# Kernel tuning notes

Measured on AMD Instinct MI355X. Metric: run time of the kernel, lower is better.

Reference implementation:

```python
import jax, jax.numpy as jnp
import numpy as np
import math

EPS_LN = 1e-5
TARGET_ACTIVITY = 0.1
THETA = 2.0 ** 16

B, NH, T, D, N = 2, 12, 2048, 768, 256


def layernorm(x):
    m = jnp.mean(x, axis=-1, keepdims=True)
    v = jnp.mean((x - m) ** 2, axis=-1, keepdims=True)
    return (x - m) / jnp.sqrt(v + EPS_LN)


def get_freqs(n):
    q = jnp.floor(jnp.arange(n, dtype=jnp.float32) / 2.0) * 2.0  # quantize by 2
    return 1.0 / (THETA ** (q / n)) / (2.0 * math.pi)


def rope(phases, v):
    ph = (phases % 1.0) * (2.0 * math.pi)
    c, s = jnp.cos(ph), jnp.sin(ph)
    even = v[..., 0::2]
    odd = v[..., 1::2]
    v_rot = jnp.stack((-odd, even), axis=-1).reshape(v.shape)  # interleaved rotate
    return v * c + v_rot * s


def setup_inputs() -> dict:
    key = jax.random.key(0)
    ks = jax.random.split(key, 5)
    std = 0.02
    return {
        "x": jax.random.normal(ks[0], (B, 1, T, D), dtype=jnp.float32),
        "encoder": jax.random.normal(ks[1], (NH, D, N), dtype=jnp.float32) * std,
        "encoder_v": jax.random.normal(ks[2], (NH, D, N), dtype=jnp.float32) * std,
        "decoder": jax.random.normal(ks[3], (NH * N, D), dtype=jnp.float32) * std,
        "scale": jnp.ones((D,), dtype=jnp.float32),
        "running_activity": jnp.ones((D,), dtype=jnp.float32) * TARGET_ACTIVITY,
    }


def reference(x, encoder, encoder_v, decoder, scale, running_activity):
    Bv, _, Tv, Dv = x.shape
    nh, _, Nv = encoder.shape

    # encode + ReLU sparsify: [B,1,T,D] @ [nh,D,N] -> [B,nh,T,N]
    x_latent = jnp.einsum('bztd,hdn->bhtn', x, encoder)
    x_sparse = jax.nn.relu(x_latent)

    # RoPE on Q=K=x_sparse
    freqs = get_freqs(Nv)  # [N]
    r_phases = jnp.arange(Tv, dtype=jnp.float32)[:, None] * freqs[None, :]  # [T,N]
    QR = rope(r_phases, x_sparse)
    KR = rope(r_phases, x_sparse)

    # non-softmax causal attention, strictly lower-triangular (diag=-1)
    scores = jnp.einsum('bhtn,bhsn->bhts', QR, KR)
    mask = jnp.tril(jnp.ones((Tv, Tv), dtype=scores.dtype), k=-1)
    scores = scores * mask
    yKV = jnp.einsum('bhts,bsd->bhtd', scores, x[:, 0])  # V = x

    yKV = layernorm(yKV)
    y_sparse = jax.nn.relu(jnp.einsum('bhtd,hdn->bhtn', yKV, encoder_v))
    xy_sparse = x_sparse * y_sparse  # [B,nh,T,N]; dropout=0 (eval)

    # [B,nh,T,N] -> [B,1,T,nh*N] @ [nh*N,D]
    flat = jnp.transpose(xy_sparse, (0, 2, 1, 3)).reshape(Bv, 1, Tv, nh * Nv)
    yMLP = flat @ decoder

    y = layernorm(yMLP)
    regulation = TARGET_ACTIVITY / (running_activity + 1e-6)
    y = y * jnp.sqrt(regulation) * scale

    return layernorm(x + y), xy_sparse
```

## Files before the change

### kernel.cpp

```cpp
#include <hip/hip_runtime.h>
#include <math.h>

#define TT 2048
#define DD 768
#define NN 256
#define NHH 12
#define BB 2
#define CH 512

typedef unsigned short u16;
typedef __attribute__((ext_vector_type(8))) short bf16x8;
typedef __attribute__((ext_vector_type(8))) unsigned short u16x8;
typedef __attribute__((ext_vector_type(4))) float f32x4;

static inline int imin(int a, int b) { return a < b ? a : b; }

__device__ __forceinline__ u16 f2b(float f) {
  union { float f; unsigned u; } a; a.f = f;
  unsigned r = a.u + 0x7FFF + ((a.u >> 16) & 1);
  return (u16)(r >> 16);
}
__device__ __forceinline__ float b2f(u16 h) {
  union { unsigned u; float f; } a; a.u = ((unsigned)h) << 16;
  return a.f;
}

__device__ __forceinline__ void async16(const void* g, void* l) {
  __builtin_amdgcn_global_load_lds(
      (const __attribute__((address_space(1))) unsigned*)g,
      (__attribute__((address_space(3))) unsigned*)l, 16, 0, 0);
}

__device__ __forceinline__ void stage128x32(
    const u16* __restrict__ gbase, size_t ld, u16* lds, int tid) {
  const int w = tid >> 6, l = tid & 63;
  const int r = l >> 2, kc = (l & 3) << 3;
#pragma unroll
  for (int q = 0; q < 2; ++q) {
    const int row0 = w * 32 + q * 16;
    async16(gbase + (size_t)(row0 + r) * ld + kc, lds + row0 * 32);
  }
}

__device__ __forceinline__ void stage64x32(
    const u16* __restrict__ gbase, size_t ld, u16* lds, int tid) {
  const int w = tid >> 6, l = tid & 63;
  const int r = w * 16 + (l >> 2), kc = (l & 3) << 3;
  async16(gbase + (size_t)r * ld + kc, lds + w * 512);
}

__device__ __forceinline__ void mfma_step(
    const u16* As, const u16* Bs, int wr, int wc, int lane, f32x4 acc[4][4]) {
  const int m16 = lane & 15, quad = lane >> 4;
  bf16x8 a[4], b[4];
#pragma unroll
  for (int i = 0; i < 4; ++i)
    a[i] = *(const bf16x8*)&As[(wr * 64 + i * 16 + m16) * 32 + quad * 8];
#pragma unroll
  for (int j = 0; j < 4; ++j)
    b[j] = *(const bf16x8*)&Bs[(wc * 64 + j * 16 + m16) * 32 + quad * 8];
#pragma unroll
  for (int i = 0; i < 4; ++i)
#pragma unroll
    for (int j = 0; j < 4; ++j)
      acc[i][j] = __builtin_amdgcn_mfma_f32_16x16x32_bf16(a[i], b[j], acc[i][j], 0, 0, 0);
}

__device__ __forceinline__ void copy_out128(
    const u16* buf, u16* g, size_t ld, int tid) {
#pragma unroll
  for (int s = 0; s < 8; ++s) {
    const int off = (s * 256 + tid) * 8;
    const int row = off >> 7, col = off & 127;
    *(u16x8*)&g[(size_t)row * ld + col] = *(const u16x8*)&buf[off];
  }
}

#define GEMM_PROLOGUE()                                            \
  __shared__ __attribute__((aligned(16))) u16 smem[16384];         \
  const int tid = threadIdx.x;                                     \
  const int w = tid >> 6, lane = tid & 63;                         \
  const int wr = w >> 1, wc = w & 1;                               \
  const int col16 = lane & 15, quad = lane >> 4;                   \
  f32x4 acc[4][4];                                                 \
  _Pragma("unroll") for (int i = 0; i < 4; ++i)                    \
  _Pragma("unroll") for (int j = 0; j < 4; ++j)                    \
      acc[i][j] = (f32x4){0.f, 0.f, 0.f, 0.f};

#define PIPELINED_K_LOOP(ABASE, ALD, BBASE, BLD, KTOT)                      \
  {                                                                         \
    u16* bA_ = smem; u16* bB_ = smem + 8192;                                \
    stage128x32((ABASE), (ALD), bA_, tid);                                  \
    stage128x32((BBASE), (BLD), bA_ + 4096, tid);                           \
    const int nk_ = (KTOT) / 32;                                            \
    for (int kp_ = 0; kp_ < nk_; ++kp_) {                                   \
      u16* cb_ = (kp_ & 1) ? bB_ : bA_;                                     \
      u16* nb_ = (kp_ & 1) ? bA_ : bB_;                                     \
      if (kp_ + 1 < nk_) {                                                  \
        const int kn_ = (kp_ + 1) * 32;                                     \
        stage128x32((ABASE) + kn_, (ALD), nb_, tid);                        \
        stage128x32((BBASE) + kn_, (BLD), nb_ + 4096, tid);                 \
        asm volatile("s_waitcnt vmcnt(4)" ::: "memory");                    \
      } else {                                                              \
        asm volatile("s_waitcnt vmcnt(0)" ::: "memory");                    \
      }                                                                     \
      __builtin_amdgcn_s_barrier();                                         \
      __builtin_amdgcn_sched_barrier(0);                                    \
      mfma_step(cb_, cb_ + 4096, wr, wc, lane, acc);                        \
      __builtin_amdgcn_sched_barrier(0);                                    \
      __builtin_amdgcn_s_barrier();                                         \
    }                                                                       \
  }

__global__ __launch_bounds__(256) void cvt_bf16(
    const float* __restrict__ in, u16* __restrict__ out, size_t n4) {
  size_t i = ((size_t)blockIdx.x * 256 + threadIdx.x) * 4;
  if (i >= n4 * 4) return;
  float4 v = *(const float4*)&in[i];
  u16 o[4] = {f2b(v.x), f2b(v.y), f2b(v.z), f2b(v.w)};
  *(ushort4*)&out[i] = *(ushort4*)o;
}

__global__ __launch_bounds__(256) void tcvt_bf16(
    const float* __restrict__ in, u16* __restrict__ out, int R, int C,
    size_t inStride, size_t outStride) {
  __shared__ float tile[32][33];
  const float* ip = in + (size_t)blockIdx.z * inStride;
  u16* op = out + (size_t)blockIdx.z * outStride;
  const int c0 = blockIdx.x * 32, r0 = blockIdx.y * 32;
  const int tx = threadIdx.x & 31, ty = threadIdx.x >> 5;
#pragma unroll
  for (int p = 0; p < 4; ++p)
    tile[ty + p * 8][tx] = ip[(size_t)(r0 + ty + p * 8) * C + c0 + tx];
  __syncthreads();
#pragma unroll
  for (int p = 0; p < 4; ++p)
    op[(size_t)(c0 + ty + p * 8) * R + r0 + tx] = f2b(tile[tx][ty + p * 8]);
}

__global__ __launch_bounds__(256) void k_colsum(
    const u16* __restrict__ encvt, float* __restrict__ colsum) {
  const int row = blockIdx.x * 4 + (threadIdx.x >> 6);
  const int lane = threadIdx.x & 63;
  const u16* pr = encvt + (size_t)row * DD;
  float s = 0.f;
#pragma unroll
  for (int i = 0; i < 3; ++i) {
    ushort4 v = *(const ushort4*)&pr[(lane << 2) + i * 256];
    s += b2f(v.x) + b2f(v.y) + b2f(v.z) + b2f(v.w);
  }
#pragma unroll
  for (int off = 32; off; off >>= 1) s += __shfl_xor(s, off);
  if (lane == 0) colsum[row] = s;
}

__global__ __launch_bounds__(256) void k_cstab(float2* __restrict__ cs) {
  const int idx = blockIdx.x * 256 + threadIdx.x;
  const int t = idx >> 7, n2 = idx & 127;
  const float freq = exp2f((float)(2 * n2) * -0.0625f) * 0.15915494309189535f;
  const float phase = (float)t * freq;
  const float ph = (phase - floorf(phase)) * 6.283185307179586f;
  cs[idx] = make_float2(__cosf(ph), __sinf(ph));
}

__global__ __launch_bounds__(256) void k1_encode(
    const u16* __restrict__ x16, const u16* __restrict__ enct,
    const float2* __restrict__ CS,
    u16* __restrict__ qr16, u16* __restrict__ qrt16) {
  const int h = blockIdx.z;
  const int m0 = blockIdx.x * 128, n0 = blockIdx.y * 128;
  GEMM_PROLOGUE();
  PIPELINED_K_LOOP(x16 + (size_t)m0 * DD, DD,
                   enct + ((size_t)h * NN + n0) * DD, DD, DD);
  __syncthreads();
#pragma unroll
  for (int i = 0; i < 4; ++i)
#pragma unroll
    for (int j = 0; j < 4; ++j) {
      const int n = n0 + wc * 64 + j * 16 + col16;
      float rv[4], pv[4];
#pragma unroll
      for (int r = 0; r < 4; ++r) rv[r] = fmaxf(acc[i][j][r], 0.f);
#pragma unroll
      for (int r = 0; r < 4; ++r) pv[r] = __shfl_xor(rv[r], 1);
#pragma unroll
      for (int r = 0; r < 4; ++r) {
        const int lrow = wr * 64 + i * 16 + quad * 4 + r;
        const int t = (m0 + lrow) & (TT - 1);
        const float2 cs = CS[t * 128 + (n >> 1)];
        const float o = (n & 1) ? (rv[r] * cs.x + pv[r] * cs.y)
                                : (rv[r] * cs.x - pv[r] * cs.y);
        smem[lrow * 128 + wc * 64 + j * 16 + col16] = f2b(o);
      }
    }
  __syncthreads();
  const int bq = m0 >> 11, tb = m0 & (TT - 1);
  const size_t sl = (size_t)(bq * NHH + h);
  copy_out128(smem, qr16 + (sl * TT + tb) * NN + n0, NN, tid);
#pragma unroll
  for (int s = 0; s < 8; ++s) {
    const int off = (s * 256 + tid) * 8;
    const int nr = off >> 7, tc = off & 127;
    u16 vals[8];
#pragma unroll
    for (int k = 0; k < 8; ++k) vals[k] = smem[(tc + k) * 128 + nr];
    *(u16x8*)&qrt16[(sl * NN + n0 + nr) * TT + tb + tc] = *(u16x8*)vals;
  }
}

__global__ __launch_bounds__(256) void kS_band(
    const u16* __restrict__ qr16, u16* __restrict__ sb, int bh0) {
  const int z = blockIdx.y;
  const int bh = bh0 + z;
  const int cc = blockIdx.x / 10, rr = blockIdx.x % 10;
  int i = (int)((sqrtf(8.f * rr + 1.f) - 1.f) * 0.5f);
  while ((i + 1) * (i + 2) / 2 <= rr) ++i;
  while (i * (i + 1) / 2 > rr) --i;
  const int j = rr - i * (i + 1) / 2;
  const int t0 = (cc * 4 + i) * 128;
  const int s0 = cc * CH + j * 128;
  const u16* q = qr16 + (size_t)bh * TT * NN;
  GEMM_PROLOGUE();
  PIPELINED_K_LOOP(q + (size_t)t0 * NN, NN, q + (size_t)s0 * NN, NN, NN);
  const bool diag = (i == j);
  __syncthreads();
#pragma unroll
  for (int ii = 0; ii < 4; ++ii)
#pragma unroll
    for (int jj = 0; jj < 4; ++jj) {
      const int s = s0 + wc * 64 + jj * 16 + col16;
#pragma unroll
      for (int r = 0; r < 4; ++r) {
        const int lrow = wr * 64 + ii * 16 + quad * 4 + r;
        const int t = t0 + lrow;
        float v = acc[ii][jj][r];
        if (diag && s >= t) v = 0.f;
        smem[lrow * 128 + wc * 64 + jj * 16 + col16] = f2b(v);
      }
    }
  __syncthreads();
  copy_out128(smem, sb + ((size_t)z * TT + t0) * CH + j * 128, CH, tid);
}

__global__ __launch_bounds__(256) void kB_all(
    const u16* __restrict__ xt16, const u16* __restrict__ qrt16,
    u16* __restrict__ h16, int bh0) {
  __shared__ __attribute__((aligned(16))) u16 sm[20480];
  u16* buf0 = sm;
  u16* buf1 = sm + 6144;
  u16* snap = sm + 12288;
  const int tid = threadIdx.x;
  const int w = tid >> 6, lane = tid & 63;
  const int m16 = lane & 15, quad = lane >> 4;
  const int z = blockIdx.z;
  const int bh = bh0 + z, b = bh / NHH;
  const int d0 = blockIdx.x * 64, n0 = blockIdx.y * 128;
  f32x4 acc[4][2];
#pragma unroll
  for (int i = 0; i < 4; ++i)
#pragma unroll
    for (int j = 0; j < 2; ++j) acc[i][j] = (f32x4){0.f, 0.f, 0.f, 0.f};
  const u16* Ab = xt16 + ((size_t)b * DD + d0) * TT;
  const u16* Bb = qrt16 + ((size_t)bh * NN + n0) * TT;
  for (int c = 0; c < 3; ++c) {
    const int kbase = c * CH;
    stage64x32(Ab + kbase, TT, buf0, tid);
    stage128x32(Bb + kbase, TT, buf0 + 2048, tid);
    for (int s = 0; s < CH / 32; ++s) {
      u16* cb = (s & 1) ? buf1 : buf0;
      u16* nb = (s & 1) ? buf0 : buf1;
      if (s + 1 < CH / 32) {
        const int kn = kbase + (s + 1) * 32;
        stage64x32(Ab + kn, TT, nb, tid);
        stage128x32(Bb + kn, TT, nb + 2048, tid);
        asm volatile("s_waitcnt vmcnt(3)" ::: "memory");
      } else {
        asm volatile("s_waitcnt vmcnt(0)" ::: "memory");
      }
      __builtin_amdgcn_s_barrier();
      __builtin_amdgcn_sched_barrier(0);
      bf16x8 a[4], bb[2];
#pragma unroll
      for (int i = 0; i < 4; ++i)
        a[i] = *(const bf16x8*)&cb[(i * 16 + m16) * 32 + quad * 8];
#pragma unroll
      for (int j = 0; j < 2; ++j)
        bb[j] = *(const bf16x8*)&cb[2048 + (w * 32 + j * 16 + m16) * 32 + quad * 8];
#pragma unroll
      for (int i = 0; i < 4; ++i)
#pragma unroll
        for (int j = 0; j < 2; ++j)
          acc[i][j] = __builtin_amdgcn_mfma_f32_16x16x32_bf16(a[i], bb[j], acc[i][j], 0, 0, 0);
      __builtin_amdgcn_sched_barrier(0);
      __builtin_amdgcn_s_barrier();
    }
#pragma unroll
    for (int i = 0; i < 4; ++i)
#pragma unroll
      for (int j = 0; j < 2; ++j)
#pragma unroll
        for (int r = 0; r < 4; ++r)
          snap[(i * 16 + quad * 4 + r) * 128 + w * 32 + j * 16 + m16] =
              f2b(acc[i][j][r]);
    __syncthreads();
    u16* hd = h16 + (size_t)(z * 3 + c) * DD * NN;
#pragma unroll
    for (int s4 = 0; s4 < 4; ++s4) {
      const int off = (s4 * 256 + tid) * 8;
      const int row = off >> 7, col = off & 127;
      *(u16x8*)&hd[(size_t)(d0 + row) * NN + n0 + col] = *(const u16x8*)&snap[off];
    }
    __syncthreads();
  }
}

__device__ static const int TTORD[16] = {15, 11, 7, 14, 10, 6, 13, 9,
                                         5, 3, 12, 8, 4, 2, 1, 0};

__global__ __launch_bounds__(256) void kA_attn(
    const u16* __restrict__ qr16, const u16* __restrict__ h16,
    const u16* __restrict__ sb, const u16* __restrict__ xt16,
    u16* __restrict__ ykv16, int bh0) {
  __shared__ __attribute__((aligned(16))) u16 smem[32768];
  const int tid = threadIdx.x;
  const int w = tid >> 6, lane = tid & 63;
  const int wr = w >> 1, wc = w & 1;
  const int col16 = lane & 15, quad = lane >> 4;
  const int nwg = gridDim.x;
  const int bid = blockIdx.x;
  const int qq = nwg >> 3, r8 = nwg & 7;
  const int xcd = bid & 7, pos = bid >> 3;
  const int wg = (xcd < r8 ? xcd * (qq + 1) : r8 * (qq + 1) + (xcd - r8) * qq) + pos;
  const int z = wg / 96;
  const int tt = TTORD[(wg / 6) & 15];
  const int d0 = (wg % 6) * 128;
  const int bh = bh0 + z, b = bh / NHH;
  const int c = tt >> 2, it = tt & 3;
  const int t0 = tt * 128;
  f32x4 acc[4][4];
#pragma unroll
  for (int i = 0; i < 4; ++i)
#pragma unroll
    for (int j = 0; j < 4; ++j) acc[i][j] = (f32x4){0.f, 0.f, 0.f, 0.f};

  const int c4 = (c > 0) ? 4 : 0;
  const int nP = c4 + (it + 1) * 2;
  const u16* hs = h16 + ((size_t)(z * 3 + (c > 0 ? c - 1 : 0)) * DD + d0) * NN;
  const u16* qb = qr16 + ((size_t)bh * TT + t0) * NN;
  const u16* sbb = sb + ((size_t)z * TT + t0) * CH;
  const u16* xb = xt16 + ((size_t)b * DD + d0) * TT + c * CH;

#define KA_STAGE(buf, p)                                                  \
  {                                                                       \
    const u16 *pa_, *pb_; size_t la_, lb_;                                \
    if ((p) < c4) {                                                       \
      pa_ = qb + (p) * 64; la_ = NN;                                      \
      pb_ = hs + (p) * 64; lb_ = NN;                                      \
    } else {                                                              \
      const int q_ = (p) - c4;                                            \
      const int j_ = q_ >> 1, kk_ = (q_ & 1) << 6;                        \
      pa_ = sbb + j_ * 128 + kk_; la_ = CH;                               \
      pb_ = xb + j_ * 128 + kk_; lb_ = TT;                                \
    }                                                                     \
    stage128x32(pa_, la_, (buf), tid);                                    \
    stage128x32(pa_ + 32, la_, (buf) + 4096, tid);                        \
    stage128x32(pb_, lb_, (buf) + 8192, tid);                             \
    stage128x32(pb_ + 32, lb_, (buf) + 12288, tid);                       \
  }

  u16* bufA = smem;
  u16* bufB = smem + 16384;
  KA_STAGE(bufA, 0);
  for (int p = 0; p < nP; ++p) {
    u16* cb = (p & 1) ? bufB : bufA;
    u16* nb = (p & 1) ? bufA : bufB;
    if (p + 1 < nP) {
      KA_STAGE(nb, p + 1);
      asm volatile("s_waitcnt vmcnt(8)" ::: "memory");
    } else {
      asm volatile("s_waitcnt vmcnt(0)" ::: "memory");
    }
    __builtin_amdgcn_s_barrier();
    __builtin_amdgcn_sched_barrier(0);
    mfma_step(cb, cb + 8192, wr, wc, lane, acc);
    mfma_step(cb + 4096, cb + 12288, wr, wc, lane, acc);
    __builtin_amdgcn_sched_barrier(0);
    __builtin_amdgcn_s_barrier();
  }
#undef KA_STAGE

  __syncthreads();
#pragma unroll
  for (int i = 0; i < 4; ++i)
#pragma unroll
    for (int j = 0; j < 4; ++j)
#pragma unroll
      for (int r = 0; r < 4; ++r) {
        const int lrow = wr * 64 + i * 16 + quad * 4 + r;
        smem[lrow * 128 + wc * 64 + j * 16 + col16] = f2b(acc[i][j][r]);
      }
  __syncthreads();
  copy_out128(smem, ykv16 + ((size_t)z * TT + t0) * DD + d0, DD, tid);
}

__global__ __launch_bounds__(256) void k3_stats(
    const u16* __restrict__ ykv16, float* __restrict__ mu, float* __restrict__ rs) {
  const int row = blockIdx.x * 4 + (threadIdx.x >> 6);
  const int lane = threadIdx.x & 63;
  const u16* p = ykv16 + (size_t)row * DD;
  float sum = 0.f, sq = 0.f;
#pragma unroll
  for (int i = 0; i < 3; ++i) {
    ushort4 v = *(const ushort4*)&p[(lane << 2) + i * 256];
    float f0 = b2f(v.x), f1 = b2f(v.y), f2 = b2f(v.z), f3 = b2f(v.w);
    sum += f0 + f1 + f2 + f3;
    sq += f0 * f0 + f1 * f1 + f2 * f2 + f3 * f3;
  }
#pragma unroll
  for (int off = 32; off; off >>= 1) {
    sum += __shfl_xor(sum, off);
    sq += __shfl_xor(sq, off);
  }
  if (lane == 0) {
    float m = sum * (1.f / 768.f);
    float v = sq * (1.f / 768.f) - m * m;
    mu[row] = m;
    rs[row] = rsqrtf(v + 1e-5f);
  }
}

__global__ __launch_bounds__(256) void k4_xy(
    const u16* __restrict__ ykv16, const u16* __restrict__ encvt,
    const float2* __restrict__ CS,
    u16* __restrict__ qrxy, const float* __restrict__ mu,
    const float* __restrict__ rs, const float* __restrict__ colsum,
    float* __restrict__ out2, int bh0) {
  const int z = blockIdx.z;
  const int bh = bh0 + z, h = bh % NHH;
  const int t0 = blockIdx.x * 128, n0 = blockIdx.y * 128;
  GEMM_PROLOGUE();
  PIPELINED_K_LOOP(ykv16 + ((size_t)z * TT + t0) * DD, DD,
                   encvt + ((size_t)h * NN + n0) * DD, DD, DD);
  __syncthreads();
#pragma unroll
  for (int i = 0; i < 4; ++i) {
    float muv[4], rsv[4];
#pragma unroll
    for (int r = 0; r < 4; ++r) {
      const int lrow = z * TT + t0 + wr * 64 + i * 16 + quad * 4 + r;
      muv[r] = mu[lrow];
      rsv[r] = rs[lrow];
    }
#pragma unroll
    for (int j = 0; j < 4; ++j) {
      const int n = n0 + wc * 64 + j * 16 + col16;
      const float csum = colsum[h * NN + n];
#pragma unroll
      for (int r = 0; r < 4; ++r) {
        const int lrow = wr * 64 + i * 16 + quad * 4 + r;
        const int t = t0 + lrow;
        const float ys = fmaxf(rsv[r] * acc[i][j][r] - rsv[r] * muv[r] * csum, 0.f);
        const size_t gi = ((size_t)bh * TT + t) * NN + n;
        const unsigned pq = *(const unsigned*)&qrxy[gi & ~(size_t)1];
        const float lo = b2f((u16)pq), hi = b2f((u16)(pq >> 16));
        const float2 cs = CS[t * 128 + (n >> 1)];
        const float xs = (n & 1) ? (hi * cs.x - lo * cs.y)
                                 : (lo * cs.x + hi * cs.y);
        const float val = ys * xs;
        out2[gi] = val;
        smem[lrow * 128 + wc * 64 + j * 16 + col16] = f2b(val);
      }
    }
  }
  __syncthreads();
  copy_out128(smem, qrxy + ((size_t)bh * TT + t0) * NN + n0, NN, tid);
}

__global__ __launch_bounds__(256) void k5_mlp(
    const u16* __restrict__ xyq, const u16* __restrict__ dect,
    float* __restrict__ ymlp) {
  __shared__ __attribute__((aligned(16))) u16 sm[16384];
  u16* buf0 = sm;
  u16* buf1 = sm + 8192;
  const int tid = threadIdx.x;
  const int w = tid >> 6, lane = tid & 63;
  const int wr = w >> 1, wc = w & 1;
  const int m16 = lane & 15, quad = lane >> 4;
  const int m0 = blockIdx.x * 64, d0 = blockIdx.y * 64;
  f32x4 acc[2][2];
#pragma unroll
  for (int i = 0; i < 2; ++i)
#pragma unroll
    for (int j = 0; j < 2; ++j) acc[i][j] = (f32x4){0.f, 0.f, 0.f, 0.f};
  const int ar = w * 16 + (lane >> 2);
  const int m = m0 + ar;
  const int b = m >> 11, t = m & (TT - 1);
  const int kc = (lane & 3) << 3;
#define K5_STAGE(buf, k0)                                                   \
  {                                                                         \
    const int hh_ = (k0) >> 8;                                              \
    const int kk_ = ((k0) & 255) + kc;                                      \
    const u16* ap_ = xyq + ((size_t)(b * NHH + hh_) * TT + t) * NN;         \
    async16(ap_ + kk_, (buf) + w * 512);                                    \
    async16(ap_ + kk_ + 32, (buf) + 2048 + w * 512);                        \
    stage64x32(dect + (size_t)d0 * (NHH * NN) + (k0), NHH * NN,             \
               (buf) + 4096, tid);                                          \
    stage64x32(dect + (size_t)d0 * (NHH * NN) + (k0) + 32, NHH * NN,        \
               (buf) + 6144, tid);                                          \
  }
  const int NK = (NHH * NN) / 64;
  K5_STAGE(buf0, 0);
  for (int s = 0; s < NK; ++s) {
    u16* cb = (s & 1) ? buf1 : buf0;
    u16* nb = (s & 1) ? buf0 : buf1;
    if (s + 1 < NK) {
      K5_STAGE(nb, (s + 1) * 64);
      asm volatile("s_waitcnt vmcnt(4)" ::: "memory");
    } else {
      asm volatile("s_waitcnt vmcnt(0)" ::: "memory");
    }
    __builtin_amdgcn_s_barrier();
    __builtin_amdgcn_sched_barrier(0);
#pragma unroll
    for (int half = 0; half < 2; ++half) {
      bf16x8 a[2], bb[2];
#pragma unroll
      for (int i = 0; i < 2; ++i)
        a[i] = *(const bf16x8*)&cb[half * 2048 + (wr * 32 + i * 16 + m16) * 32 + quad * 8];
#pragma unroll
      for (int j = 0; j < 2; ++j)
        bb[j] = *(const bf16x8*)&cb[4096 + half * 2048 + (wc * 32 + j * 16 + m16) * 32 + quad * 8];
#pragma unroll
      for (int i = 0; i < 2; ++i)
#pragma unroll
        for (int j = 0; j < 2; ++j)
          acc[i][j] = __builtin_amdgcn_mfma_f32_16x16x32_bf16(a[i], bb[j], acc[i][j], 0, 0, 0);
    }
    __builtin_amdgcn_sched_barrier(0);
    __builtin_amdgcn_s_barrier();
  }
#undef K5_STAGE
#pragma unroll
  for (int i = 0; i < 2; ++i)
#pragma unroll
    for (int j = 0; j < 2; ++j) {
      const int d = d0 + wc * 32 + j * 16 + m16;
#pragma unroll
      for (int r = 0; r < 4; ++r) {
        const int mm = m0 + wr * 32 + i * 16 + quad * 4 + r;
        ymlp[(size_t)mm * DD + d] = acc[i][j][r];
      }
    }
}

__global__ __launch_bounds__(256) void k6_final(
    const float* __restrict__ ymlp, const float* __restrict__ x,
    const float* __restrict__ scale, const float* __restrict__ ra,
    float* __restrict__ out1) {
  const int row = blockIdx.x;
  const int tid = threadIdx.x;
  const int wid = tid >> 6, lane = tid & 63;
  __shared__ float red[8];
  float v[3];
  float sum = 0.f, sq = 0.f;
#pragma unroll
  for (int j = 0; j < 3; ++j) {
    v[j] = ymlp[(size_t)row * DD + tid + j * 256];
    sum += v[j]; sq += v[j] * v[j];
  }
#pragma unroll
  for (int off = 32; off; off >>= 1) { sum += __shfl_xor(sum, off); sq += __shfl_xor(sq, off); }
  if (lane == 0) { red[wid] = sum; red[4 + wid] = sq; }
  __syncthreads();
  sum = red[0] + red[1] + red[2] + red[3];
  sq = red[4] + red[5] + red[6] + red[7];
  const float m1 = sum * (1.f / 768.f);
  const float r1 = rsqrtf(sq * (1.f / 768.f) - m1 * m1 + 1e-5f);
  float z[3];
  float sum2 = 0.f, sq2 = 0.f;
#pragma unroll
  for (int j = 0; j < 3; ++j) {
    const int d = tid + j * 256;
    float y = (v[j] - m1) * r1 * sqrtf(0.1f / (ra[d] + 1e-6f)) * scale[d];
    z[j] = x[(size_t)row * DD + d] + y;
    sum2 += z[j]; sq2 += z[j] * z[j];
  }
  __syncthreads();
#pragma unroll
  for (int off = 32; off; off >>= 1) { sum2 += __shfl_xor(sum2, off); sq2 += __shfl_xor(sq2, off); }
  if (lane == 0) { red[wid] = sum2; red[4 + wid] = sq2; }
  __syncthreads();
  sum2 = red[0] + red[1] + red[2] + red[3];
  sq2 = red[4] + red[5] + red[6] + red[7];
  const float m2 = sum2 * (1.f / 768.f);
  const float r2 = rsqrtf(sq2 * (1.f / 768.f) - m2 * m2 + 1e-5f);
#pragma unroll
  for (int j = 0; j < 3; ++j)
    out1[(size_t)row * DD + tid + j * 256] = (z[j] - m2) * r2;
}

extern "C" void kernel_launch(void* const* d_in, const int* in_sizes, int n_in,
                              void* d_out, int out_size, void* d_ws, size_t ws_size,
                              hipStream_t stream) {
  const float* x = (const float*)d_in[0];
  const float* enc = (const float*)d_in[1];
  const float* encv = (const float*)d_in[2];
  const float* dec = (const float*)d_in[3];
  const float* scale = (const float*)d_in[4];
  const float* ra = (const float*)d_in[5];
  float* out1 = (float*)d_out;
  float* out2 = out1 + (size_t)BB * TT * DD;
  float* ymlp = out1;

  const int NS = BB * NHH;
  unsigned char* p = (unsigned char*)d_ws;
  u16* X16 = (u16*)p;    p += (size_t)BB * TT * DD * 2;
  u16* XT16 = (u16*)p;   p += (size_t)BB * DD * TT * 2;
  u16* ENCT = (u16*)p;   p += (size_t)NHH * NN * DD * 2;
  u16* ENCVT = (u16*)p;  p += (size_t)NHH * NN * DD * 2;
  u16* DECT = (u16*)p;   p += (size_t)DD * NHH * NN * 2;
  u16* QR16 = (u16*)p;   p += (size_t)NS * TT * NN * 2;
  u16* QRT16 = (u16*)p;  p += (size_t)NS * NN * TT * 2;
  float* COLSUM = (float*)p; p += (size_t)NHH * NN * 4;
  float2* CS = (float2*)p;   p += (size_t)TT * (NN / 2) * sizeof(float2);
  const size_t SLICE_B = (size_t)TT * CH * 2 + 3 * (size_t)DD * NN * 2 +
                         (size_t)TT * DD * 2 + (size_t)TT * 8;
  size_t fixed = (size_t)(p - (unsigned char*)d_ws);
  size_t rem = (ws_size > fixed) ? ws_size - fixed : 0;
  int GSmax = (int)(rem / SLICE_B);
  if (GSmax < 1) GSmax = 1;
  if (GSmax > NS) GSmax = NS;
  const int ngrp = (NS + GSmax - 1) / GSmax;
  const int GS = (NS + ngrp - 1) / ngrp;
  u16* SB = (u16*)p;     p += (size_t)GS * TT * CH * 2;
  u16* H16 = (u16*)p;    p += (size_t)GS * 3 * DD * NN * 2;
  u16* YKV16 = (u16*)p;  p += (size_t)GS * TT * DD * 2;
  float* MU = (float*)p; p += (size_t)GS * TT * 4;
  float* RS = (float*)p; p += (size_t)GS * TT * 4;

  cvt_bf16<<<dim3((BB * TT * DD) / 1024), 256, 0, stream>>>(x, X16, (size_t)BB * TT * DD / 4);
  tcvt_bf16<<<dim3(DD / 32, TT / 32, BB), 256, 0, stream>>>(
      x, XT16, TT, DD, (size_t)TT * DD, (size_t)DD * TT);
  tcvt_bf16<<<dim3(NN / 32, DD / 32, NHH), 256, 0, stream>>>(
      enc, ENCT, DD, NN, (size_t)DD * NN, (size_t)NN * DD);
  tcvt_bf16<<<dim3(NN / 32, DD / 32, NHH), 256, 0, stream>>>(
      encv, ENCVT, DD, NN, (size_t)DD * NN, (size_t)NN * DD);
  tcvt_bf16<<<dim3(DD / 32, (NHH * NN) / 32, 1), 256, 0, stream>>>(
      dec, DECT, NHH * NN, DD, 0, 0);
  k_colsum<<<dim3(NHH * NN / 4), 256, 0, stream>>>(ENCVT, COLSUM);
  k_cstab<<<dim3(TT * (NN / 2) / 256), 256, 0, stream>>>(CS);

  k1_encode<<<dim3(BB * TT / 128, NN / 128, NHH), 256, 0, stream>>>(
      X16, ENCT, CS, QR16, QRT16);

  for (int bh0 = 0; bh0 < NS; bh0 += GS) {
    const int gs = imin(GS, NS - bh0);
    kS_band<<<dim3(40, gs), 256, 0, stream>>>(QR16, SB, bh0);
    kB_all<<<dim3(DD / 64, NN / 128, gs), 256, 0, stream>>>(
        XT16, QRT16, H16, bh0);
    kA_attn<<<dim3(96 * gs), 256, 0, stream>>>(
        QR16, H16, SB, XT16, YKV16, bh0);
    k3_stats<<<dim3(gs * TT / 4), 256, 0, stream>>>(YKV16, MU, RS);
    k4_xy<<<dim3(TT / 128, NN / 128, gs), 256, 0, stream>>>(
        YKV16, ENCVT, CS, QR16, MU, RS, COLSUM, out2, bh0);
  }

  k5_mlp<<<dim3(BB * TT / 64, DD / 64), 256, 0, stream>>>(QR16, DECT, ymlp);
  k6_final<<<dim3(BB * TT), 256, 0, stream>>>(ymlp, x, scale, ra, out1);
}
```

Measured before the change: 402.3 us.

## Deepen K-step per stage to 64 and triple-buffer MLP GEMM

The shared GEMM pipeline now stages 64-wide K slices (two 32-wide sub-tiles per operand) per double-buffered step, halving barrier and wait rounds in the encode, band, and yKV-encode kernels; kB_all does the same. The MLP kernel switches to a three-stage rotating buffer so two loads are in flight ahead of compute. The encode epilogue XOR-swizzles its LDS staging to reduce bank conflicts on the transposed readout. The cost is roughly double the LDS per block, which may reduce occupancy.

```diff
diff --git a/kernel.cpp b/kernel.cpp
--- a/kernel.cpp
+++ b/kernel.cpp
@@ -77,7 +77,7 @@
 }
 
 #define GEMM_PROLOGUE()                                            \
-  __shared__ __attribute__((aligned(16))) u16 smem[16384];         \
+  __shared__ __attribute__((aligned(16))) u16 smem[32768];         \
   const int tid = threadIdx.x;                                     \
   const int w = tid >> 6, lane = tid & 63;                         \
   const int wr = w >> 1, wc = w & 1;                               \
@@ -87,26 +87,30 @@
   _Pragma("unroll") for (int j = 0; j < 4; ++j)                    \
       acc[i][j] = (f32x4){0.f, 0.f, 0.f, 0.f};
 
-#define PIPELINED_K_LOOP(ABASE, ALD, BBASE, BLD, KTOT)                      \
+#define PIPELINED_K_LOOP64(ABASE, ALD, BBASE, BLD, KTOT)                    \
   {                                                                         \
-    u16* bA_ = smem; u16* bB_ = smem + 8192;                                \
-    stage128x32((ABASE), (ALD), bA_, tid);                                  \
-    stage128x32((BBASE), (BLD), bA_ + 4096, tid);                           \
-    const int nk_ = (KTOT) / 32;                                            \
-    for (int kp_ = 0; kp_ < nk_; ++kp_) {                                   \
-      u16* cb_ = (kp_ & 1) ? bB_ : bA_;                                     \
-      u16* nb_ = (kp_ & 1) ? bA_ : bB_;                                     \
-      if (kp_ + 1 < nk_) {                                                  \
-        const int kn_ = (kp_ + 1) * 32;                                     \
+    stage128x32((ABASE), (ALD), smem, tid);                                 \
+    stage128x32((ABASE) + 32, (ALD), smem + 4096, tid);                     \
+    stage128x32((BBASE), (BLD), smem + 8192, tid);                          \
+    stage128x32((BBASE) + 32, (BLD), smem + 12288, tid);                    \
+    const int np_ = (KTOT) / 64;                                            \
+    for (int pp_ = 0; pp_ < np_; ++pp_) {                                   \
+      u16* cb_ = (pp_ & 1) ? smem + 16384 : smem;                           \
+      u16* nb_ = (pp_ & 1) ? smem : smem + 16384;                           \
+      if (pp_ + 1 < np_) {                                                  \
+        const int kn_ = (pp_ + 1) * 64;                                     \
         stage128x32((ABASE) + kn_, (ALD), nb_, tid);                        \
-        stage128x32((BBASE) + kn_, (BLD), nb_ + 4096, tid);                 \
-        asm volatile("s_waitcnt vmcnt(4)" ::: "memory");                    \
+        stage128x32((ABASE) + kn_ + 32, (ALD), nb_ + 4096, tid);            \
+        stage128x32((BBASE) + kn_, (BLD), nb_ + 8192, tid);                 \
+        stage128x32((BBASE) + kn_ + 32, (BLD), nb_ + 12288, tid);           \
+        asm volatile("s_waitcnt vmcnt(8)" ::: "memory");                    \
       } else {                                                              \
         asm volatile("s_waitcnt vmcnt(0)" ::: "memory");                    \
       }                                                                     \
       __builtin_amdgcn_s_barrier();                                         \
       __builtin_amdgcn_sched_barrier(0);                                    \
-      mfma_step(cb_, cb_ + 4096, wr, wc, lane, acc);                        \
+      mfma_step(cb_, cb_ + 8192, wr, wc, lane, acc);                        \
+      mfma_step(cb_ + 4096, cb_ + 12288, wr, wc, lane, acc);                \
       __builtin_amdgcn_sched_barrier(0);                                    \
       __builtin_amdgcn_s_barrier();                                         \
     }                                                                       \
@@ -163,6 +167,8 @@
   cs[idx] = make_float2(__cosf(ph), __sinf(ph));
 }
 
+__device__ __forceinline__ int swz8(int row) { return ((row >> 3) & 7) << 3; }
+
 __global__ __launch_bounds__(256) void k1_encode(
     const u16* __restrict__ x16, const u16* __restrict__ enct,
     const float2* __restrict__ CS,
@@ -170,8 +176,8 @@
   const int h = blockIdx.z;
   const int m0 = blockIdx.x * 128, n0 = blockIdx.y * 128;
   GEMM_PROLOGUE();
-  PIPELINED_K_LOOP(x16 + (size_t)m0 * DD, DD,
-                   enct + ((size_t)h * NN + n0) * DD, DD, DD);
+  PIPELINED_K_LOOP64(x16 + (size_t)m0 * DD, DD,
+                     enct + ((size_t)h * NN + n0) * DD, DD, DD);
   __syncthreads();
 #pragma unroll
   for (int i = 0; i < 4; ++i)
@@ -190,20 +196,28 @@
         const float2 cs = CS[t * 128 + (n >> 1)];
         const float o = (n & 1) ? (rv[r] * cs.x + pv[r] * cs.y)
                                 : (rv[r] * cs.x - pv[r] * cs.y);
-        smem[lrow * 128 + wc * 64 + j * 16 + col16] = f2b(o);
+        smem[lrow * 128 + ((wc * 64 + j * 16 + col16) ^ swz8(lrow))] = f2b(o);
       }
     }
   __syncthreads();
   const int bq = m0 >> 11, tb = m0 & (TT - 1);
   const size_t sl = (size_t)(bq * NHH + h);
-  copy_out128(smem, qr16 + (sl * TT + tb) * NN + n0, NN, tid);
+  u16* qg = qr16 + (sl * TT + tb) * NN + n0;
+#pragma unroll
+  for (int s = 0; s < 8; ++s) {
+    const int off = (s * 256 + tid) * 8;
+    const int row = off >> 7, col = off & 127;
+    *(u16x8*)&qg[(size_t)row * NN + col] =
+        *(const u16x8*)&smem[row * 128 + (col ^ swz8(row))];
+  }
 #pragma unroll
   for (int s = 0; s < 8; ++s) {
     const int off = (s * 256 + tid) * 8;
     const int nr = off >> 7, tc = off & 127;
+    const int sw = swz8(tc);
     u16 vals[8];
 #pragma unroll
-    for (int k = 0; k < 8; ++k) vals[k] = smem[(tc + k) * 128 + nr];
+    for (int k = 0; k < 8; ++k) vals[k] = smem[(tc + k) * 128 + (nr ^ sw)];
     *(u16x8*)&qrt16[(sl * NN + n0 + nr) * TT + tb + tc] = *(u16x8*)vals;
   }
 }
@@ -221,7 +235,7 @@
   const int s0 = cc * CH + j * 128;
   const u16* q = qr16 + (size_t)bh * TT * NN;
   GEMM_PROLOGUE();
-  PIPELINED_K_LOOP(q + (size_t)t0 * NN, NN, q + (size_t)s0 * NN, NN, NN);
+  PIPELINED_K_LOOP64(q + (size_t)t0 * NN, NN, q + (size_t)s0 * NN, NN, NN);
   const bool diag = (i == j);
   __syncthreads();
 #pragma unroll
@@ -245,10 +259,10 @@
 __global__ __launch_bounds__(256) void kB_all(
     const u16* __restrict__ xt16, const u16* __restrict__ qrt16,
     u16* __restrict__ h16, int bh0) {
-  __shared__ __attribute__((aligned(16))) u16 sm[20480];
+  __shared__ __attribute__((aligned(16))) u16 sm[32768];
   u16* buf0 = sm;
-  u16* buf1 = sm + 6144;
-  u16* snap = sm + 12288;
+  u16* buf1 = sm + 12288;
+  u16* snap = sm + 24576;
   const int tid = threadIdx.x;
   const int w = tid >> 6, lane = tid & 63;
   const int m16 = lane & 15, quad = lane >> 4;
@@ -262,35 +276,43 @@
     for (int j = 0; j < 2; ++j) acc[i][j] = (f32x4){0.f, 0.f, 0.f, 0.f};
   const u16* Ab = xt16 + ((size_t)b * DD + d0) * TT;
   const u16* Bb = qrt16 + ((size_t)bh * NN + n0) * TT;
+#define KB_STAGE(buf, k0)                                                   \
+  {                                                                         \
+    stage64x32(Ab + (k0), TT, (buf), tid);                                  \
+    stage64x32(Ab + (k0) + 32, TT, (buf) + 2048, tid);                      \
+    stage128x32(Bb + (k0), TT, (buf) + 4096, tid);                          \
+    stage128x32(Bb + (k0) + 32, TT, (buf) + 8192, tid);                     \
+  }
   for (int c = 0; c < 3; ++c) {
     const int kbase = c * CH;
-    stage64x32(Ab + kbase, TT, buf0, tid);
-    stage128x32(Bb + kbase, TT, buf0 + 2048, tid);
-    for (int s = 0; s < CH / 32; ++s) {
+    KB_STAGE(buf0, kbase);
+    for (int s = 0; s < CH / 64; ++s) {
       u16* cb = (s & 1) ? buf1 : buf0;
       u16* nb = (s & 1) ? buf0 : buf1;
-      if (s + 1 < CH / 32) {
-        const int kn = kbase + (s + 1) * 32;
-        stage64x32(Ab + kn, TT, nb, tid);
-        stage128x32(Bb + kn, TT, nb + 2048, tid);
-        asm volatile("s_waitcnt vmcnt(3)" ::: "memory");
+      if (s + 1 < CH / 64) {
+        KB_STAGE(nb, kbase + (s + 1) * 64);
+        asm volatile("s_waitcnt vmcnt(6)" ::: "memory");
       } else {
         asm volatile("s_waitcnt vmcnt(0)" ::: "memory");
       }
       __builtin_amdgcn_s_barrier();
       __builtin_amdgcn_sched_barrier(0);
-      bf16x8 a[4], bb[2];
-#pragma unroll
-      for (int i = 0; i < 4; ++i)
-        a[i] = *(const bf16x8*)&cb[(i * 16 + m16) * 32 + quad * 8];
-#pragma unroll
-      for (int j = 0; j < 2; ++j)
-        bb[j] = *(const bf16x8*)&cb[2048 + (w * 32 + j * 16 + m16) * 32 + quad * 8];
-#pragma unroll
-      for (int i = 0; i < 4; ++i)
+#pragma unroll
+      for (int half = 0; half < 2; ++half) {
+        bf16x8 a[4], bb[2];
+#pragma unroll
+        for (int i = 0; i < 4; ++i)
+          a[i] = *(const bf16x8*)&cb[half * 2048 + (i * 16 + m16) * 32 + quad * 8];
 #pragma unroll
         for (int j = 0; j < 2; ++j)
-          acc[i][j] = __builtin_amdgcn_mfma_f32_16x16x32_bf16(a[i], bb[j], acc[i][j], 0, 0, 0);
+          bb[j] = *(const bf16x8*)&cb[4096 + half * 4096 +
+                                      (w * 32 + j * 16 + m16) * 32 + quad * 8];
+#pragma unroll
+        for (int i = 0; i < 4; ++i)
+#pragma unroll
+          for (int j = 0; j < 2; ++j)
+            acc[i][j] = __builtin_amdgcn_mfma_f32_16x16x32_bf16(a[i], bb[j], acc[i][j], 0, 0, 0);
+      }
       __builtin_amdgcn_sched_barrier(0);
       __builtin_amdgcn_s_barrier();
     }
@@ -312,6 +334,7 @@
     }
     __syncthreads();
   }
+#undef KB_STAGE
 }
 
 __device__ static const int TTORD[16] = {15, 11, 7, 14, 10, 6, 13, 9,
@@ -439,8 +462,8 @@
   const int bh = bh0 + z, h = bh % NHH;
   const int t0 = blockIdx.x * 128, n0 = blockIdx.y * 128;
   GEMM_PROLOGUE();
-  PIPELINED_K_LOOP(ykv16 + ((size_t)z * TT + t0) * DD, DD,
-                   encvt + ((size_t)h * NN + n0) * DD, DD, DD);
+  PIPELINED_K_LOOP64(ykv16 + ((size_t)z * TT + t0) * DD, DD,
+                     encvt + ((size_t)h * NN + n0) * DD, DD, DD);
   __syncthreads();
 #pragma unroll
   for (int i = 0; i < 4; ++i) {
@@ -479,9 +502,7 @@
 __global__ __launch_bounds__(256) void k5_mlp(
     const u16* __restrict__ xyq, const u16* __restrict__ dect,
     float* __restrict__ ymlp) {
-  __shared__ __attribute__((aligned(16))) u16 sm[16384];
-  u16* buf0 = sm;
-  u16* buf1 = sm + 8192;
+  __shared__ __attribute__((aligned(16))) u16 sm[24576];
   const int tid = threadIdx.x;
   const int w = tid >> 6, lane = tid & 63;
   const int wr = w >> 1, wc = w & 1;
@@ -509,12 +530,14 @@
                (buf) + 6144, tid);                                          \
   }
   const int NK = (NHH * NN) / 64;
-  K5_STAGE(buf0, 0);
+  u16 *b0 = sm, *b1 = sm + 8192, *b2 = sm + 16384;
+  K5_STAGE(b0, 0);
+  K5_STAGE(b1, 64);
   for (int s = 0; s < NK; ++s) {
-    u16* cb = (s & 1) ? buf1 : buf0;
-    u16* nb = (s & 1) ? buf0 : buf1;
-    if (s + 1 < NK) {
-      K5_STAGE(nb, (s + 1) * 64);
+    if (s + 2 < NK) {
+      K5_STAGE(b2, (s + 2) * 64);
+      asm volatile("s_waitcnt vmcnt(8)" ::: "memory");
+    } else if (s + 1 < NK) {
       asm volatile("s_waitcnt vmcnt(4)" ::: "memory");
     } else {
       asm volatile("s_waitcnt vmcnt(0)" ::: "memory");
@@ -526,10 +549,10 @@
       bf16x8 a[2], bb[2];
 #pragma unroll
       for (int i = 0; i < 2; ++i)
-        a[i] = *(const bf16x8*)&cb[half * 2048 + (wr * 32 + i * 16 + m16) * 32 + quad * 8];
+        a[i] = *(const bf16x8*)&b0[half * 2048 + (wr * 32 + i * 16 + m16) * 32 + quad * 8];
 #pragma unroll
       for (int j = 0; j < 2; ++j)
-        bb[j] = *(const bf16x8*)&cb[4096 + half * 2048 + (wc * 32 + j * 16 + m16) * 32 + quad * 8];
+        bb[j] = *(const bf16x8*)&b0[4096 + half * 2048 + (wc * 32 + j * 16 + m16) * 32 + quad * 8];
 #pragma unroll
       for (int i = 0; i < 2; ++i)
 #pragma unroll
@@ -538,6 +561,7 @@
     }
     __builtin_amdgcn_sched_barrier(0);
     __builtin_amdgcn_s_barrier();
+    u16* tmp = b0; b0 = b1; b1 = b2; b2 = tmp;
   }
 #undef K5_STAGE
 #pragma unroll
```

Measured after the change: 379.9 us. -5.6%, faster.
